# Optimization experiments

Measured on AMD Instinct MI355X. Metric: run time of the kernel, lower is better.

The kernel has to match this reference:

```python
import jax, jax.numpy as jnp
import numpy as np

N, IN_DIM, UNITS, Z_DEPTH, Z_K = 8192, 1024, 512, 32, 256


def setup_inputs() -> dict:
    key = jax.random.key(0)
    ks = jax.random.split(key, 10)
    s = 0.02
    return {
        "x": jax.random.normal(ks[0], (N, IN_DIM), jnp.float32),
        "h_W": jax.random.normal(ks[1], (IN_DIM, UNITS), jnp.float32) * s,
        "h_U": jax.random.normal(ks[2], (UNITS, UNITS), jnp.float32) * s,
        "h_b": jnp.zeros((UNITS,), jnp.float32),
        "f_W": jax.random.normal(ks[3], (UNITS, UNITS), jnp.float32) * s,
        "f_b": jnp.zeros((UNITS,), jnp.float32),
        "i_W": jax.random.normal(ks[4], (UNITS, UNITS), jnp.float32) * s,
        "i_b": jnp.zeros((UNITS,), jnp.float32),
        "c_W": jax.random.normal(ks[5], (UNITS, UNITS), jnp.float32) * s,
        "c_b": jnp.zeros((UNITS,), jnp.float32),
        "o_W": jax.random.normal(ks[6], (UNITS, UNITS), jnp.float32) * s,
        "o_b": jnp.zeros((UNITS,), jnp.float32),
        "t_W": jax.random.normal(ks[7], (UNITS, UNITS), jnp.float32) * s,
        "t_b": jnp.zeros((UNITS,), jnp.float32),
        "y_W": jax.random.normal(ks[8], (UNITS, Z_K), jnp.float32) * s,
        "y_b": jnp.zeros((Z_K,), jnp.float32),
        "h0": jnp.zeros((1, UNITS), jnp.float32),
        "z_depth": Z_DEPTH,
    }


def reference(x, h_W, h_U, h_b, f_W, f_b, i_W, i_b, c_W, c_b, o_W, o_b,
              t_W, t_b, y_W, y_b, h0, z_depth):
    n = x.shape[0]
    # x @ h_W is the same every step; hoist it out of the scan.
    xh = x @ h_W + h_b  # [n, units]

    def step(h_prev, _):
        h = jnp.tanh(xh + h_prev @ h_U)
        f = jax.nn.sigmoid(h @ f_W + f_b)
        i = jax.nn.sigmoid(h @ i_W + i_b)
        c = jnp.tanh(h @ c_W + c_b)
        o = jax.nn.sigmoid(h @ o_W + o_b)
        h1 = h_prev * f + c * i
        t = jnp.tanh((o * h1) @ t_W + t_b)
        y = jnp.tanh(t @ y_W + y_b)  # activation=tanh
        return h1, y

    h_init = jnp.broadcast_to(h0, (n, h0.shape[1]))
    _, ys = jax.lax.scan(step, h_init, None, length=z_depth)  # ys: [z_depth, n, z_k]
    return jnp.transpose(ys, (1, 0, 2))  # [n, z_depth, z_k]
```

## Files before the change

kernel.cpp:

```cpp
#include <hip/hip_runtime.h>


typedef _Float16 half_t;
typedef _Float16 half8 __attribute__((ext_vector_type(8)));
typedef _Float16 half4v __attribute__((ext_vector_type(4)));
typedef float float4_ __attribute__((ext_vector_type(4)));

#define UNITS 512
#define IN_DIM 1024
#define NROWS 8192
#define DEPTH 32
#define ZK 256
#define MT 32
#define PITCH (UNITS + 8)
#define XPITCH (IN_DIM + 8)

__device__ inline float4_ mfma16(half8 a, half8 b, float4_ c) {
  return __builtin_amdgcn_mfma_f32_16x16x32_f16(a, b, c, 0, 0, 0);
}
__device__ inline float fast_sigmoid(float x) {
  return __builtin_amdgcn_rcpf(1.0f + __builtin_amdgcn_exp2f(-1.4426950408889634f * x));
}
__device__ inline float fast_tanh(float x) {
  return 2.0f * __builtin_amdgcn_rcpf(1.0f + __builtin_amdgcn_exp2f(-2.8853900817779268f * x)) - 1.0f;
}

template<int NM, class OffF>
__device__ inline void sweepW(const half_t* __restrict__ wbase, OffF off,
                              const half_t* __restrict__ abase,
                              float4_ (&acc)[NM][2]) {
#pragma unroll
  for (int i = 0; i < NM; ++i) {
    acc[i][0] = {0.f, 0.f, 0.f, 0.f};
    acc[i][1] = {0.f, 0.f, 0.f, 0.f};
  }
  half8 w0[3][NM], w1[3][NM];
#pragma unroll
  for (int sl = 0; sl < 2; ++sl)
#pragma unroll
    for (int i = 0; i < NM; ++i) {
      w0[sl][i] = *(const half8*)(wbase + off(i) + sl * 64);
      w1[sl][i] = *(const half8*)(wbase + off(i) + sl * 64 + 32);
    }
#pragma unroll
  for (int kk = 0; kk < 8; ++kk) {
    const int cur = kk % 3;
    if (kk < 6) {
      const int pf = (kk + 2) % 3;
      const int kpf = (kk + 2) * 64;
#pragma unroll
      for (int i = 0; i < NM; ++i) {
        w0[pf][i] = *(const half8*)(wbase + off(i) + kpf);
        w1[pf][i] = *(const half8*)(wbase + off(i) + kpf + 32);
      }
    }
    const int k0 = kk * 64;
    half8 a00 = *(const half8*)(abase + k0);
    half8 a01 = *(const half8*)(abase + k0 + 32);
    half8 a10 = *(const half8*)(abase + 16 * PITCH + k0);
    half8 a11 = *(const half8*)(abase + 16 * PITCH + k0 + 32);
#pragma unroll
    for (int i = 0; i < NM; ++i) {
      acc[i][0] = mfma16(w0[cur][i], a00, acc[i][0]);
      acc[i][0] = mfma16(w1[cur][i], a01, acc[i][0]);
      acc[i][1] = mfma16(w0[cur][i], a10, acc[i][1]);
      acc[i][1] = mfma16(w1[cur][i], a11, acc[i][1]);
    }
  }
}

template<int NB, int K, int AP, class OffF>
__device__ inline void stage_gemm(const half_t* __restrict__ bbase, OffF off,
                                  const half_t* __restrict__ A, int q, int c16,
                                  float4_ (&acc)[NB][2]) {
#pragma unroll
  for (int nb = 0; nb < NB; ++nb) {
    acc[nb][0] = {0.f, 0.f, 0.f, 0.f};
    acc[nb][1] = {0.f, 0.f, 0.f, 0.f};
  }
  for (int k0 = 0; k0 < K; k0 += 64) {
    const half_t* ap = A + c16 * AP + k0 + q * 8;
    half8 a00 = *(const half8*)(ap);
    half8 a01 = *(const half8*)(ap + 32);
    half8 a10 = *(const half8*)(ap + 16 * AP);
    half8 a11 = *(const half8*)(ap + 16 * AP + 32);
#pragma unroll
    for (int nb = 0; nb < NB; ++nb) {
      const half_t* bp = bbase + off(nb) + k0;
      half8 b0 = *(const half8*)(bp);
      half8 b1 = *(const half8*)(bp + 32);
      acc[nb][0] = mfma16(a00, b0, acc[nb][0]);
      acc[nb][0] = mfma16(a01, b1, acc[nb][0]);
      acc[nb][1] = mfma16(a10, b0, acc[nb][1]);
      acc[nb][1] = mfma16(a11, b1, acc[nb][1]);
    }
  }
}

__global__ void transpose_convert(const float* __restrict__ in, half_t* __restrict__ out,
                                  int R, int C) {
  __shared__ float tile[32][33];
  int c0 = blockIdx.x * 32, r0 = blockIdx.y * 32;
  int tx = threadIdx.x, ty = threadIdx.y;
#pragma unroll
  for (int i = 0; i < 32; i += 8)
    tile[ty + i][tx] = in[(size_t)(r0 + ty + i) * C + c0 + tx];
  __syncthreads();
#pragma unroll
  for (int i = 0; i < 32; i += 8)
    out[(size_t)(c0 + ty + i) * R + r0 + tx] = (half_t)tile[tx][ty + i];
}

__global__ __launch_bounds__(512, 2) void xh_kernel(
    const float* __restrict__ x, const half_t* __restrict__ hW_T,
    const float* __restrict__ h_b, half_t* __restrict__ xh_g) {
  extern __shared__ half_t sx[];
  const int tid = threadIdx.x;
  const int w = tid >> 6, l = tid & 63, q = l >> 4, c16 = l & 15;
  const int row0 = blockIdx.x * 32;
  for (int it = tid; it < 32 * IN_DIM / 4; it += 512) {
    int r = it >> 8;
    int c = (it & 255) * 4;
    float4_ v = __builtin_nontemporal_load((const float4_*)(x + (size_t)(row0 + r) * IN_DIM + c));
    half4v hv;
    hv[0] = (half_t)v[0]; hv[1] = (half_t)v[1]; hv[2] = (half_t)v[2]; hv[3] = (half_t)v[3];
    *(half4v*)(sx + r * XPITCH + c) = hv;
  }
  __syncthreads();
  const int n0 = w * 64;
  float4_ acc[4][2];
  const half_t* bbase = hW_T + (size_t)(n0 + c16) * IN_DIM + q * 8;
  stage_gemm<4, IN_DIM, XPITCH>(bbase, [](int nb) { return nb * 16 * IN_DIM; }, sx, q, c16, acc);
#pragma unroll
  for (int nb = 0; nb < 4; ++nb)
#pragma unroll
    for (int mb = 0; mb < 2; ++mb)
#pragma unroll
      for (int r = 0; r < 4; ++r) {
        int row = mb * 16 + q * 4 + r;
        int col = n0 + nb * 16 + c16;
        xh_g[(size_t)(row0 + row) * UNITS + col] = (half_t)(acc[nb][mb][r] + h_b[col]);
      }
}

__global__ __launch_bounds__(512, 2) void lstm_main(
    const half_t* __restrict__ xh_g, const half_t* __restrict__ hU_T,
    const half_t* __restrict__ W4_T, const half_t* __restrict__ tW_T,
    const half_t* __restrict__ yW_T,
    const float* __restrict__ f_b, const float* __restrict__ i_b,
    const float* __restrict__ c_b, const float* __restrict__ o_b,
    const float* __restrict__ t_b, const float* __restrict__ y_b,
    const float* __restrict__ h0, float* __restrict__ out) {
  extern __shared__ half_t smem[];
  half_t* bufA = smem;
  half_t* bufB = smem + MT * PITCH;
  half_t* s_xh = smem + 2 * MT * PITCH;
  float* s_bias = (float*)(smem + 3 * MT * PITCH);
  float* s_fb = s_bias;
  float* s_ib = s_bias + 512;
  float* s_cb = s_bias + 1024;
  float* s_ob = s_bias + 1536;
  float* s_tb = s_bias + 2048;
  float* s_yb = s_bias + 2560;

  const int tid = threadIdx.x;
  const int w = tid >> 6, l = tid & 63, q = l >> 4, c16 = l & 15;
  const int row0 = blockIdx.x * MT;

  for (int it = tid; it < MT * UNITS / 8; it += 512) {
    int r = it >> 6;
    int c = (it & 63) * 8;
    float4_ v0 = *(const float4_*)(h0 + c);
    float4_ v1 = *(const float4_*)(h0 + c + 4);
    half8 hv;
#pragma unroll
    for (int j = 0; j < 4; ++j) { hv[j] = (half_t)v0[j]; hv[4 + j] = (half_t)v1[j]; }
    *(half8*)(bufA + r * PITCH + c) = hv;
    *(half8*)(s_xh + r * PITCH + c) = *(const half8*)(xh_g + (size_t)(row0 + r) * UNITS + c);
  }
  for (int it = tid; it < 512; it += 512) {
    s_fb[it] = f_b[it]; s_ib[it] = i_b[it]; s_cb[it] = c_b[it]; s_ob[it] = o_b[it];
    s_tb[it] = t_b[it];
    if (it < 256) s_yb[it] = y_b[it];
  }
  half4v state_r[2][2][2];
#pragma unroll
  for (int hh = 0; hh < 2; ++hh)
#pragma unroll
    for (int cm = 0; cm < 2; ++cm) {
      int col0 = hh * 256 + w * 32 + cm * 16 + q * 4;
      float4_ v = *(const float4_*)(h0 + col0);
      half4v s4;
#pragma unroll
      for (int r = 0; r < 4; ++r) s4[r] = (half_t)v[r];
#pragma unroll
      for (int rb = 0; rb < 2; ++rb) state_r[hh][cm][rb] = s4;
    }
  __syncthreads();

  for (int s = 0; s < DEPTH; ++s) {
    {
      float4_ acc[4][2];
      const half_t* wb = hU_T + (size_t)(w * 64 + c16) * UNITS + q * 8;
      sweepW<4>(wb, [](int i) { return i * 16 * UNITS; }, bufA + c16 * PITCH + q * 8, acc);
#pragma unroll
      for (int cm = 0; cm < 4; ++cm) {
        int col0 = w * 64 + cm * 16 + q * 4;
#pragma unroll
        for (int rb = 0; rb < 2; ++rb) {
          int row = rb * 16 + c16;
          half4v xh4 = *(const half4v*)(s_xh + row * PITCH + col0);
          half4v hv;
#pragma unroll
          for (int r = 0; r < 4; ++r) hv[r] = (half_t)fast_tanh(acc[cm][rb][r] + (float)xh4[r]);
          *(half4v*)(bufB + row * PITCH + col0) = hv;
        }
      }
    }
    __syncthreads();
#pragma unroll 1
    for (int hh = 0; hh < 2; ++hh) {
      float4_ acc[8][2];
      const int colbase = hh * 256 + w * 32;
      const half_t* wb = W4_T + (size_t)(colbase + c16) * UNITS + q * 8;
      sweepW<8>(wb, [](int i) { return (i >> 1) * (UNITS * UNITS) + (i & 1) * 16 * UNITS; },
                bufB + c16 * PITCH + q * 8, acc);
#pragma unroll
      for (int cm = 0; cm < 2; ++cm) {
        int col0 = colbase + cm * 16 + q * 4;
        float4_ fb4 = *(const float4_*)(s_fb + col0);
        float4_ ib4 = *(const float4_*)(s_ib + col0);
        float4_ cb4 = *(const float4_*)(s_cb + col0);
        float4_ ob4 = *(const float4_*)(s_ob + col0);
#pragma unroll
        for (int rb = 0; rb < 2; ++rb) {
          int row = rb * 16 + c16;
          half4v hp = state_r[hh][cm][rb];
          half4v h1v, sbv;
#pragma unroll
          for (int r = 0; r < 4; ++r) {
            float gf = fast_sigmoid(acc[0 * 2 + cm][rb][r] + fb4[r]);
            float gi = fast_sigmoid(acc[1 * 2 + cm][rb][r] + ib4[r]);
            float gc = fast_tanh   (acc[2 * 2 + cm][rb][r] + cb4[r]);
            float go = fast_sigmoid(acc[3 * 2 + cm][rb][r] + ob4[r]);
            float h1 = (float)hp[r] * gf + gc * gi;
            h1v[r] = (half_t)h1;
            sbv[r] = (half_t)(go * h1);
          }
          state_r[hh][cm][rb] = h1v;
          *(half4v*)(bufA + row * PITCH + col0) = sbv;
        }
      }
    }
    __syncthreads();
    {
      float4_ acc[4][2];
      const half_t* wb = tW_T + (size_t)(w * 64 + c16) * UNITS + q * 8;
      sweepW<4>(wb, [](int i) { return i * 16 * UNITS; }, bufA + c16 * PITCH + q * 8, acc);
#pragma unroll
      for (int cm = 0; cm < 4; ++cm) {
        int col0 = w * 64 + cm * 16 + q * 4;
        float4_ tb4 = *(const float4_*)(s_tb + col0);
#pragma unroll
        for (int rb = 0; rb < 2; ++rb) {
          int row = rb * 16 + c16;
          half4v hv;
#pragma unroll
          for (int r = 0; r < 4; ++r) hv[r] = (half_t)fast_tanh(acc[cm][rb][r] + tb4[r]);
          *(half4v*)(bufB + row * PITCH + col0) = hv;
        }
      }
    }
    __syncthreads();
    {
      float4_ acc[2][2];
      const half_t* wb = yW_T + (size_t)(w * 32 + c16) * UNITS + q * 8;
      sweepW<2>(wb, [](int i) { return i * 16 * UNITS; }, bufB + c16 * PITCH + q * 8, acc);
#pragma unroll
      for (int cm = 0; cm < 2; ++cm) {
        int col0 = w * 32 + cm * 16 + q * 4;
        float4_ yb4 = *(const float4_*)(s_yb + col0);
#pragma unroll
        for (int rb = 0; rb < 2; ++rb) {
          int row = rb * 16 + c16;
          float4_ yv;
#pragma unroll
          for (int r = 0; r < 4; ++r) yv[r] = fast_tanh(acc[cm][rb][r] + yb4[r]);
          __builtin_nontemporal_store(yv,
              (float4_*)(out + ((size_t)(row0 + row) * DEPTH + s) * ZK + col0));
        }
      }
#pragma unroll
      for (int hh = 0; hh < 2; ++hh)
#pragma unroll
        for (int cm = 0; cm < 2; ++cm) {
          int col0 = hh * 256 + w * 32 + cm * 16 + q * 4;
#pragma unroll
          for (int rb = 0; rb < 2; ++rb)
            *(half4v*)(bufA + (rb * 16 + c16) * PITCH + col0) = state_r[hh][cm][rb];
        }
    }
    __syncthreads();
  }
}

extern "C" void kernel_launch(void* const* d_in, const int* in_sizes, int n_in,
                              void* d_out, int out_size, void* d_ws, size_t ws_size,
                              hipStream_t stream) {
  (void)in_sizes; (void)n_in; (void)out_size; (void)ws_size;
  const float* x   = (const float*)d_in[0];
  const float* h_W = (const float*)d_in[1];
  const float* h_U = (const float*)d_in[2];
  const float* h_b = (const float*)d_in[3];
  const float* f_W = (const float*)d_in[4];
  const float* f_b = (const float*)d_in[5];
  const float* i_W = (const float*)d_in[6];
  const float* i_b = (const float*)d_in[7];
  const float* c_W = (const float*)d_in[8];
  const float* c_b = (const float*)d_in[9];
  const float* o_W = (const float*)d_in[10];
  const float* o_b = (const float*)d_in[11];
  const float* t_W = (const float*)d_in[12];
  const float* t_b = (const float*)d_in[13];
  const float* y_W = (const float*)d_in[14];
  const float* y_b = (const float*)d_in[15];
  const float* h0  = (const float*)d_in[16];
  float* out = (float*)d_out;

  half_t* ws   = (half_t*)d_ws;
  half_t* hW_T = ws;
  half_t* hU_T = hW_T + (size_t)UNITS * IN_DIM;
  half_t* W4_T = hU_T + (size_t)UNITS * UNITS;
  half_t* tW_T = W4_T + (size_t)4 * UNITS * UNITS;
  half_t* yW_T = tW_T + (size_t)UNITS * UNITS;
  half_t* xh_g = yW_T + (size_t)ZK * UNITS;

  const int lds_main = 3 * MT * PITCH * 2 + 2816 * 4;
  hipFuncSetAttribute((const void*)xh_kernel, hipFuncAttributeMaxDynamicSharedMemorySize,
                      32 * XPITCH * 2);
  hipFuncSetAttribute((const void*)lstm_main, hipFuncAttributeMaxDynamicSharedMemorySize,
                      lds_main);

  dim3 tb(32, 8);
  hipLaunchKernelGGL(transpose_convert, dim3(UNITS / 32, IN_DIM / 32), tb, 0, stream,
                     h_W, hW_T, IN_DIM, UNITS);
  hipLaunchKernelGGL(transpose_convert, dim3(UNITS / 32, UNITS / 32), tb, 0, stream,
                     h_U, hU_T, UNITS, UNITS);
  hipLaunchKernelGGL(transpose_convert, dim3(UNITS / 32, UNITS / 32), tb, 0, stream,
                     f_W, W4_T + 0 * (size_t)UNITS * UNITS, UNITS, UNITS);
  hipLaunchKernelGGL(transpose_convert, dim3(UNITS / 32, UNITS / 32), tb, 0, stream,
                     i_W, W4_T + 1 * (size_t)UNITS * UNITS, UNITS, UNITS);
  hipLaunchKernelGGL(transpose_convert, dim3(UNITS / 32, UNITS / 32), tb, 0, stream,
                     c_W, W4_T + 2 * (size_t)UNITS * UNITS, UNITS, UNITS);
  hipLaunchKernelGGL(transpose_convert, dim3(UNITS / 32, UNITS / 32), tb, 0, stream,
                     o_W, W4_T + 3 * (size_t)UNITS * UNITS, UNITS, UNITS);
  hipLaunchKernelGGL(transpose_convert, dim3(UNITS / 32, UNITS / 32), tb, 0, stream,
                     t_W, tW_T, UNITS, UNITS);
  hipLaunchKernelGGL(transpose_convert, dim3(ZK / 32, UNITS / 32), tb, 0, stream,
                     y_W, yW_T, UNITS, ZK);
  hipLaunchKernelGGL(xh_kernel, dim3(NROWS / 32), dim3(512), 32 * XPITCH * 2, stream,
                     x, hW_T, h_b, xh_g);
  hipLaunchKernelGGL(lstm_main, dim3(NROWS / MT), dim3(512), lds_main, stream,
                     xh_g, hU_T, W4_T, tW_T, yW_T, f_b, i_b, c_b, o_b, t_b, y_b, h0, out);
}
```

Before: 4.322 ms.

## Stream LSTM weights through double-buffered LDS ring via async global_load_lds

Replaces the register-prefetched global weight loads in every recurrent GEMM with per-wave global_load_lds transfers into a two-slot LDS ring. Each k-chunk's load is issued one chunk ahead and waited on with explicit vmcnt. The last chunk of each stage prefetches the first chunk of the next stage, including across timesteps. The xh tile moves from LDS into registers to free room for the ring. This aims to hide weight fetch latency and cut register pressure, but it depends on hand-written waitcnt counts and raises total LDS use, which may lower occupancy.

```diff
diff --git a/kernel.cpp b/kernel.cpp
--- a/kernel.cpp
+++ b/kernel.cpp
@@ -14,57 +14,66 @@
 #define MT 32
 #define PITCH (UNITS + 8)
 #define XPITCH (IN_DIM + 8)
-
-__device__ inline float4_ mfma16(half8 a, half8 b, float4_ c) {
+#define RING_H 16384
+
+__device__ __forceinline__ float4_ mfma16(half8 a, half8 b, float4_ c) {
   return __builtin_amdgcn_mfma_f32_16x16x32_f16(a, b, c, 0, 0, 0);
 }
-__device__ inline float fast_sigmoid(float x) {
+__device__ __forceinline__ float fast_sigmoid(float x) {
   return __builtin_amdgcn_rcpf(1.0f + __builtin_amdgcn_exp2f(-1.4426950408889634f * x));
 }
-__device__ inline float fast_tanh(float x) {
+__device__ __forceinline__ float fast_tanh(float x) {
   return 2.0f * __builtin_amdgcn_rcpf(1.0f + __builtin_amdgcn_exp2f(-2.8853900817779268f * x)) - 1.0f;
 }
-
-template<int NM, class OffF>
-__device__ inline void sweepW(const half_t* __restrict__ wbase, OffF off,
-                              const half_t* __restrict__ abase,
-                              float4_ (&acc)[NM][2]) {
-#pragma unroll
-  for (int i = 0; i < NM; ++i) {
-    acc[i][0] = {0.f, 0.f, 0.f, 0.f};
-    acc[i][1] = {0.f, 0.f, 0.f, 0.f};
-  }
-  half8 w0[3][NM], w1[3][NM];
-#pragma unroll
-  for (int sl = 0; sl < 2; ++sl)
-#pragma unroll
-    for (int i = 0; i < NM; ++i) {
-      w0[sl][i] = *(const half8*)(wbase + off(i) + sl * 64);
-      w1[sl][i] = *(const half8*)(wbase + off(i) + sl * 64 + 32);
-    }
-#pragma unroll
-  for (int kk = 0; kk < 8; ++kk) {
-    const int cur = kk % 3;
-    if (kk < 6) {
-      const int pf = (kk + 2) % 3;
-      const int kpf = (kk + 2) * 64;
-#pragma unroll
-      for (int i = 0; i < NM; ++i) {
-        w0[pf][i] = *(const half8*)(wbase + off(i) + kpf);
-        w1[pf][i] = *(const half8*)(wbase + off(i) + kpf + 32);
-      }
-    }
-    const int k0 = kk * 64;
-    half8 a00 = *(const half8*)(abase + k0);
-    half8 a01 = *(const half8*)(abase + k0 + 32);
-    half8 a10 = *(const half8*)(abase + 16 * PITCH + k0);
-    half8 a11 = *(const half8*)(abase + 16 * PITCH + k0 + 32);
-#pragma unroll
-    for (int i = 0; i < NM; ++i) {
-      acc[i][0] = mfma16(w0[cur][i], a00, acc[i][0]);
-      acc[i][0] = mfma16(w1[cur][i], a01, acc[i][0]);
-      acc[i][1] = mfma16(w0[cur][i], a10, acc[i][1]);
-      acc[i][1] = mfma16(w1[cur][i], a11, acc[i][1]);
+__device__ __forceinline__ void gload_lds16(const half_t* g, half_t* l) {
+  __builtin_amdgcn_global_load_lds((const __attribute__((address_space(1))) void*)g,
+                                   (__attribute__((address_space(3))) void*)l, 16, 0, 0);
+}
+
+template<class IssueF, class NextF>
+__device__ __forceinline__ void sweep32(IssueF issueK, NextF next, int wread,
+                                        half_t* sl0, const half_t* abase,
+                                        float4_ (&acc)[4][2]) {
+#pragma unroll
+  for (int kc = 0; kc < 16; ++kc) {
+    if (kc < 15) issueK(kc + 1, (kc + 1) & 1);
+    else next();
+    asm volatile("s_waitcnt vmcnt(4)" ::: "memory");
+    const half_t* wsl = sl0 + (kc & 1) * RING_H;
+    half8 wv[4];
+#pragma unroll
+    for (int j = 0; j < 4; ++j) wv[j] = *(const half8*)(wsl + j * 512 + wread);
+    half8 a0 = *(const half8*)(abase + kc * 32);
+    half8 a1 = *(const half8*)(abase + 16 * PITCH + kc * 32);
+#pragma unroll
+    for (int j = 0; j < 4; ++j) {
+      acc[j][0] = mfma16(wv[j], a0, acc[j][0]);
+      acc[j][1] = mfma16(wv[j], a1, acc[j][1]);
+    }
+  }
+}
+
+template<class IssueF, class NextF>
+__device__ __forceinline__ void sweep64y(IssueF issueK, NextF next, int wread,
+                                         half_t* sl0, const half_t* abase,
+                                         float4_ (&acc)[2][2]) {
+#pragma unroll
+  for (int kc = 0; kc < 8; ++kc) {
+    if (kc < 7) issueK(kc + 1, (kc + 1) & 1);
+    else next();
+    asm volatile("s_waitcnt vmcnt(4)" ::: "memory");
+    const half_t* wsl = sl0 + (kc & 1) * RING_H;
+    half8 wv[4];
+#pragma unroll
+    for (int j = 0; j < 4; ++j) wv[j] = *(const half8*)(wsl + j * 512 + wread);
+#pragma unroll
+    for (int rb = 0; rb < 2; ++rb) {
+      half8 ak0 = *(const half8*)(abase + rb * 16 * PITCH + kc * 64);
+      half8 ak1 = *(const half8*)(abase + rb * 16 * PITCH + kc * 64 + 32);
+      acc[0][rb] = mfma16(wv[0], ak0, acc[0][rb]);
+      acc[1][rb] = mfma16(wv[1], ak0, acc[1][rb]);
+      acc[0][rb] = mfma16(wv[2], ak1, acc[0][rb]);
+      acc[1][rb] = mfma16(wv[3], ak1, acc[1][rb]);
     }
   }
 }
@@ -154,18 +163,21 @@
   extern __shared__ half_t smem[];
   half_t* bufA = smem;
   half_t* bufB = smem + MT * PITCH;
-  half_t* s_xh = smem + 2 * MT * PITCH;
-  float* s_bias = (float*)(smem + 3 * MT * PITCH);
+  float* s_bias = (float*)(smem + 2 * MT * PITCH);
   float* s_fb = s_bias;
   float* s_ib = s_bias + 512;
   float* s_cb = s_bias + 1024;
   float* s_ob = s_bias + 1536;
   float* s_tb = s_bias + 2048;
   float* s_yb = s_bias + 2560;
+  half_t* ring = smem + 2 * MT * PITCH + 2816 * 2;
 
   const int tid = threadIdx.x;
   const int w = tid >> 6, l = tid & 63, q = l >> 4, c16 = l & 15;
   const int row0 = blockIdx.x * MT;
+  half_t* sl0 = ring + w * 2048;
+  const int laneoff = c16 * 1024 + q * 16;
+  const int wread = q * 128 + c16 * 8;
 
   for (int it = tid; it < MT * UNITS / 8; it += 512) {
     int r = it >> 6;
@@ -176,13 +188,20 @@
 #pragma unroll
     for (int j = 0; j < 4; ++j) { hv[j] = (half_t)v0[j]; hv[4 + j] = (half_t)v1[j]; }
     *(half8*)(bufA + r * PITCH + c) = hv;
-    *(half8*)(s_xh + r * PITCH + c) = *(const half8*)(xh_g + (size_t)(row0 + r) * UNITS + c);
-  }
-  for (int it = tid; it < 512; it += 512) {
+  }
+  {
+    int it = tid;
     s_fb[it] = f_b[it]; s_ib[it] = i_b[it]; s_cb[it] = c_b[it]; s_ob[it] = o_b[it];
     s_tb[it] = t_b[it];
     if (it < 256) s_yb[it] = y_b[it];
   }
+  half4v xh_r[4][2];
+#pragma unroll
+  for (int cm = 0; cm < 4; ++cm)
+#pragma unroll
+    for (int rb = 0; rb < 2; ++rb)
+      xh_r[cm][rb] = *(const half4v*)(xh_g + (size_t)(row0 + rb * 16 + c16) * UNITS +
+                                      w * 64 + cm * 16 + q * 4);
   half4v state_r[2][2][2];
 #pragma unroll
   for (int hh = 0; hh < 2; ++hh)
@@ -198,65 +217,111 @@
     }
   __syncthreads();
 
+  const char* hU_c = (const char*)hU_T;
+  const char* W4_c = (const char*)W4_T;
+  const char* tW_c = (const char*)tW_T;
+  const char* yW_c = (const char*)yW_T;
+
+  auto iss = [&](const char* g0, int b0, int b1, int b2, int b3, int buf) {
+    half_t* d = sl0 + buf * RING_H;
+    gload_lds16((const half_t*)(g0 + b0), d);
+    gload_lds16((const half_t*)(g0 + b1), d + 512);
+    gload_lds16((const half_t*)(g0 + b2), d + 1024);
+    gload_lds16((const half_t*)(g0 + b3), d + 1536);
+  };
+  const int bA0 = (w * 64) * 1024, bA1 = (w * 64 + 16) * 1024,
+            bA2 = (w * 64 + 32) * 1024, bA3 = (w * 64 + 48) * 1024;
+  auto isHU = [&](int kc, int buf) { iss(hU_c + kc * 64 + laneoff, bA0, bA1, bA2, bA3, buf); };
+  auto isTW = [&](int kc, int buf) { iss(tW_c + kc * 64 + laneoff, bA0, bA1, bA2, bA3, buf); };
+  auto s2b = [&](int hh, int p, int j) {
+    return ((2 * p + (j >> 1)) * 512 + hh * 256 + w * 32 + (j & 1) * 16) * 1024;
+  };
+  auto isW4 = [&](int hh, int p, int kc, int buf) {
+    iss(W4_c + kc * 64 + laneoff, s2b(hh, p, 0), s2b(hh, p, 1), s2b(hh, p, 2), s2b(hh, p, 3), buf);
+  };
+  const int bY0 = (w * 32) * 1024, bY1 = (w * 32 + 16) * 1024;
+  auto isYW = [&](int kc, int buf) {
+    iss(yW_c + kc * 128 + laneoff, bY0, bY1, bY0 + 64, bY1 + 64, buf);
+  };
+  auto gates = [&](int hh, float4_ (&a8)[2][4][2]) {
+#pragma unroll
+    for (int cm = 0; cm < 2; ++cm) {
+      int col0 = hh * 256 + w * 32 + cm * 16 + q * 4;
+      float4_ fb4 = *(const float4_*)(s_fb + col0);
+      float4_ ib4 = *(const float4_*)(s_ib + col0);
+      float4_ cb4 = *(const float4_*)(s_cb + col0);
+      float4_ ob4 = *(const float4_*)(s_ob + col0);
+#pragma unroll
+      for (int rb = 0; rb < 2; ++rb) {
+        int row = rb * 16 + c16;
+        half4v hp = state_r[hh][cm][rb];
+        half4v h1v, sbv;
+#pragma unroll
+        for (int r = 0; r < 4; ++r) {
+          float gf = fast_sigmoid(a8[0][cm][rb][r] + fb4[r]);
+          float gi = fast_sigmoid(a8[0][2 + cm][rb][r] + ib4[r]);
+          float gc = fast_tanh   (a8[1][cm][rb][r] + cb4[r]);
+          float go = fast_sigmoid(a8[1][2 + cm][rb][r] + ob4[r]);
+          float h1 = (float)hp[r] * gf + gc * gi;
+          h1v[r] = (half_t)h1;
+          sbv[r] = (half_t)(go * h1);
+        }
+        state_r[hh][cm][rb] = h1v;
+        *(half4v*)(bufA + row * PITCH + col0) = sbv;
+      }
+    }
+  };
+
+  isHU(0, 0);
   for (int s = 0; s < DEPTH; ++s) {
     {
       float4_ acc[4][2];
-      const half_t* wb = hU_T + (size_t)(w * 64 + c16) * UNITS + q * 8;
-      sweepW<4>(wb, [](int i) { return i * 16 * UNITS; }, bufA + c16 * PITCH + q * 8, acc);
+#pragma unroll
+      for (int i = 0; i < 4; ++i) { acc[i][0] = {0.f,0.f,0.f,0.f}; acc[i][1] = {0.f,0.f,0.f,0.f}; }
+      sweep32(isHU, [&] { isW4(0, 0, 0, 0); }, wread, sl0, bufA + c16 * PITCH + q * 8, acc);
 #pragma unroll
       for (int cm = 0; cm < 4; ++cm) {
         int col0 = w * 64 + cm * 16 + q * 4;
 #pragma unroll
         for (int rb = 0; rb < 2; ++rb) {
           int row = rb * 16 + c16;
-          half4v xh4 = *(const half4v*)(s_xh + row * PITCH + col0);
           half4v hv;
 #pragma unroll
-          for (int r = 0; r < 4; ++r) hv[r] = (half_t)fast_tanh(acc[cm][rb][r] + (float)xh4[r]);
+          for (int r = 0; r < 4; ++r)
+            hv[r] = (half_t)fast_tanh(acc[cm][rb][r] + (float)xh_r[cm][rb][r]);
           *(half4v*)(bufB + row * PITCH + col0) = hv;
         }
       }
     }
     __syncthreads();
-#pragma unroll 1
-    for (int hh = 0; hh < 2; ++hh) {
-      float4_ acc[8][2];
-      const int colbase = hh * 256 + w * 32;
-      const half_t* wb = W4_T + (size_t)(colbase + c16) * UNITS + q * 8;
-      sweepW<8>(wb, [](int i) { return (i >> 1) * (UNITS * UNITS) + (i & 1) * 16 * UNITS; },
-                bufB + c16 * PITCH + q * 8, acc);
-#pragma unroll
-      for (int cm = 0; cm < 2; ++cm) {
-        int col0 = colbase + cm * 16 + q * 4;
-        float4_ fb4 = *(const float4_*)(s_fb + col0);
-        float4_ ib4 = *(const float4_*)(s_ib + col0);
-        float4_ cb4 = *(const float4_*)(s_cb + col0);
-        float4_ ob4 = *(const float4_*)(s_ob + col0);
-#pragma unroll
-        for (int rb = 0; rb < 2; ++rb) {
-          int row = rb * 16 + c16;
-          half4v hp = state_r[hh][cm][rb];
-          half4v h1v, sbv;
-#pragma unroll
-          for (int r = 0; r < 4; ++r) {
-            float gf = fast_sigmoid(acc[0 * 2 + cm][rb][r] + fb4[r]);
-            float gi = fast_sigmoid(acc[1 * 2 + cm][rb][r] + ib4[r]);
-            float gc = fast_tanh   (acc[2 * 2 + cm][rb][r] + cb4[r]);
-            float go = fast_sigmoid(acc[3 * 2 + cm][rb][r] + ob4[r]);
-            float h1 = (float)hp[r] * gf + gc * gi;
-            h1v[r] = (half_t)h1;
-            sbv[r] = (half_t)(go * h1);
-          }
-          state_r[hh][cm][rb] = h1v;
-          *(half4v*)(bufA + row * PITCH + col0) = sbv;
-        }
-      }
+    {
+      const half_t* ab = bufB + c16 * PITCH + q * 8;
+      float4_ a8[2][4][2];
+#pragma unroll
+      for (int p = 0; p < 2; ++p)
+#pragma unroll
+        for (int i = 0; i < 4; ++i) { a8[p][i][0] = {0.f,0.f,0.f,0.f}; a8[p][i][1] = {0.f,0.f,0.f,0.f}; }
+      sweep32([&](int kc, int b) { isW4(0, 0, kc, b); }, [&] { isW4(0, 1, 0, 0); },
+              wread, sl0, ab, a8[0]);
+      sweep32([&](int kc, int b) { isW4(0, 1, kc, b); }, [&] { isW4(1, 0, 0, 0); },
+              wread, sl0, ab, a8[1]);
+      gates(0, a8);
+#pragma unroll
+      for (int p = 0; p < 2; ++p)
+#pragma unroll
+        for (int i = 0; i < 4; ++i) { a8[p][i][0] = {0.f,0.f,0.f,0.f}; a8[p][i][1] = {0.f,0.f,0.f,0.f}; }
+      sweep32([&](int kc, int b) { isW4(1, 0, kc, b); }, [&] { isW4(1, 1, 0, 0); },
+              wread, sl0, ab, a8[0]);
+      sweep32([&](int kc, int b) { isW4(1, 1, kc, b); }, [&] { isTW(0, 0); },
+              wread, sl0, ab, a8[1]);
+      gates(1, a8);
     }
     __syncthreads();
     {
       float4_ acc[4][2];
-      const half_t* wb = tW_T + (size_t)(w * 64 + c16) * UNITS + q * 8;
-      sweepW<4>(wb, [](int i) { return i * 16 * UNITS; }, bufA + c16 * PITCH + q * 8, acc);
+#pragma unroll
+      for (int i = 0; i < 4; ++i) { acc[i][0] = {0.f,0.f,0.f,0.f}; acc[i][1] = {0.f,0.f,0.f,0.f}; }
+      sweep32(isTW, [&] { isYW(0, 0); }, wread, sl0, bufA + c16 * PITCH + q * 8, acc);
 #pragma unroll
       for (int cm = 0; cm < 4; ++cm) {
         int col0 = w * 64 + cm * 16 + q * 4;
@@ -274,8 +339,9 @@
     __syncthreads();
     {
       float4_ acc[2][2];
-      const half_t* wb = yW_T + (size_t)(w * 32 + c16) * UNITS + q * 8;
-      sweepW<2>(wb, [](int i) { return i * 16 * UNITS; }, bufB + c16 * PITCH + q * 8, acc);
+#pragma unroll
+      for (int i = 0; i < 2; ++i) { acc[i][0] = {0.f,0.f,0.f,0.f}; acc[i][1] = {0.f,0.f,0.f,0.f}; }
+      sweep64y(isYW, [&] { isHU(0, 0); }, wread, sl0, bufB + c16 * PITCH + q * 8, acc);
 #pragma unroll
       for (int cm = 0; cm < 2; ++cm) {
         int col0 = w * 32 + cm * 16 + q * 4;
@@ -335,7 +401,7 @@
   half_t* yW_T = tW_T + (size_t)UNITS * UNITS;
   half_t* xh_g = yW_T + (size_t)ZK * UNITS;
 
-  const int lds_main = 3 * MT * PITCH * 2 + 2816 * 4;
+  const int lds_main = 2 * MT * PITCH * 2 + 2816 * 4 + 2 * RING_H * 2;
   hipFuncSetAttribute((const void*)xh_kernel, hipFuncAttributeMaxDynamicSharedMemorySize,
                       32 * XPITCH * 2);
   hipFuncSetAttribute((const void*)lstm_main, hipFuncAttributeMaxDynamicSharedMemorySize,
```

Measured after the change: 7.191 ms. 1.66x slower.
